# Kernel tuning notes

Hardware: AMD Instinct MI355X
Metric: run time of the kernel (lower is better)

Reference implementation:

```python
import jax, jax.numpy as jnp
import numpy as np

B, NX, NY = 16, 1024, 1024
DIN_X, DIN_Y = 768, 283
DK, DV, NH = 80, 80, 8
HK, HV = DK // NH, DV // NH  # 10, 10
NORM = 1.0 / np.sqrt(HK)


def setup_inputs() -> dict:
    key = jax.random.key(0)
    kx, ky, kq, kk, kv = jax.random.split(key, 5)
    x = jax.random.normal(kx, (B, NX, DIN_X), dtype=jnp.float32)
    y = jax.random.normal(ky, (B, NY, DIN_Y), dtype=jnp.float32)
    attn_mask = jnp.zeros((B, NX, NY), dtype=jnp.float32)  # unused in forward (dead arg in original)
    # torch nn.Linear weights are [out, in]; kaiming-uniform-ish init scale
    Wq = jax.random.normal(kq, (DK, DIN_X), dtype=jnp.float32) / np.sqrt(DIN_X)
    Wk = jax.random.normal(kk, (DK, DIN_Y), dtype=jnp.float32) / np.sqrt(DIN_Y)
    Wv = jax.random.normal(kv, (DV, DIN_Y), dtype=jnp.float32) / np.sqrt(DIN_Y)
    return {"x": x, "y": y, "attn_mask": attn_mask, "Wq": Wq, "Wk": Wk, "Wv": Wv}


def reference(x, y, attn_mask, Wq, Wk, Wv):
    b, n_x, _ = x.shape
    n_y = y.shape[1]
    # projections (Linear, no bias): [B,N,D] @ W^T
    q = (x @ Wq.T).reshape(b, n_x, NH, HK).transpose(0, 2, 1, 3)  # [B,H,Nx,hk]
    k = (y @ Wk.T).reshape(b, n_y, NH, HK).transpose(0, 2, 1, 3)  # [B,H,Ny,hk]
    v = (y @ Wv.T).reshape(b, n_y, NH, HV).transpose(0, 2, 1, 3)  # [B,H,Ny,hv]
    scores = jnp.einsum("bhqd,bhkd->bhqk", q, k) * NORM          # [B,H,Nx,Ny]
    dist = jax.nn.softmax(scores, axis=-1)
    # dropout p=0.5 is identity in eval mode
    att = jnp.einsum("bhqk,bhkd->bhqd", dist, v)                  # [B,H,Nx,hv]
    att = att.transpose(0, 2, 1, 3).reshape(b, n_x, DV)           # [B,Nx,dim_v]
    return att, dist
```

## Files before the change

kernel.cpp:

```cpp
#include <hip/hip_runtime.h>
#include <hip/hip_bf16.h>

#define BB 16
#define NXX 1024
#define NYY 1024
#define DINX 768
#define DINY 283
#define NHH 8
#define HKK 10
#define DKV 80
#define NORMF 0.31622776601683794f

#define NP 1310720UL
#define NR2 4194304UL


__device__ __forceinline__ float dot10(const float* a, const float* b) {
  float s = a[0] * b[0];
#pragma unroll
  for (int d = 1; d < 10; ++d) s = fmaf(a[d], b[d], s);
  return s;
}

__global__ __launch_bounds__(256) void proj_q(
    const float* __restrict__ X, const float* __restrict__ Wq, float* __restrict__ Pq) {
  __shared__ float Xs[64 * 33];
  const int t = threadIdx.x;
  const int rt = blockIdx.x >> 2;
  const int ks = blockIdx.x & 3;
  const int w = __builtin_amdgcn_readfirstlane(t >> 6);
  const int lane = t & 63;
  const int cbase = w * 20;
  const int kbase = ks * 192;

  float acc[20];
#pragma unroll
  for (int c = 0; c < 20; ++c) acc[c] = 0.f;

#pragma unroll 1
  for (int ch = 0; ch < 6; ++ch) {
    const int dk = kbase + ch * 32;
    __syncthreads();
    for (int u = t; u < 2048; u += 256) {
      const int r = u >> 5, c = u & 31;
      Xs[r * 33 + c] = X[(size_t)(rt * 64 + r) * DINX + dk + c];
    }
    __syncthreads();
    float xv[32];
#pragma unroll
    for (int k = 0; k < 32; ++k) xv[k] = Xs[lane * 33 + k];
#pragma unroll
    for (int c = 0; c < 20; ++c) {
      const float* wr = Wq + (size_t)(cbase + c) * DINX + dk;
#pragma unroll
      for (int k = 0; k < 32; ++k) acc[c] = fmaf(wr[k], xv[k], acc[c]);
    }
  }

  const int row = rt * 64 + lane;
  const int b = row >> 10, n = row & 1023;
  float* dst = Pq + (size_t)ks * NP;
#pragma unroll
  for (int c = 0; c < 20; ++c) {
    const int cc = cbase + c, h = cc / 10, d = cc - 10 * h;
    dst[(((size_t)b * NHH + h) * 1024 + n) * 10 + d] = acc[c];
  }
}

__global__ __launch_bounds__(512) void proj_kv(
    const float* __restrict__ Y, const float* __restrict__ WK, const float* __restrict__ WV,
    float* __restrict__ PKd, float* __restrict__ PKr) {
  __shared__ float Xs[64 * 33];
  const int t = threadIdx.x;
  const int rt = blockIdx.x >> 1;
  const int ks = blockIdx.x & 1;
  const int w = __builtin_amdgcn_readfirstlane(t >> 6);
  const int lane = t & 63;
  const bool isV = (w >= 4);
  const int cbase = (isV ? (w - 4) : w) * 20;
  const float* W = isV ? WV : WK;
  const int kbase = ks * 160;
  const int nch = ks ? 4 : 5;

  float acc[20];
#pragma unroll
  for (int c = 0; c < 20; ++c) acc[c] = 0.f;

#pragma unroll 1
  for (int ch = 0; ch < nch; ++ch) {
    const int dk = kbase + ch * 32;
    __syncthreads();
    for (int u = t; u < 2048; u += 512) {
      const int r = u >> 5, c = u & 31;
      const int d = dk + c;
      Xs[r * 33 + c] = (d < DINY) ? Y[(size_t)(rt * 64 + r) * DINY + d] : 0.f;
    }
    __syncthreads();
    float xv[32];
#pragma unroll
    for (int k = 0; k < 32; ++k) xv[k] = Xs[lane * 33 + k];
    if (dk + 32 <= DINY) {
#pragma unroll
      for (int c = 0; c < 20; ++c) {
        const float* wr = W + (size_t)(cbase + c) * DINY + dk;
#pragma unroll
        for (int k = 0; k < 32; ++k) acc[c] = fmaf(wr[k], xv[k], acc[c]);
      }
    } else {
#pragma unroll
      for (int c = 0; c < 20; ++c) {
        const float* wr = W + (size_t)(cbase + c) * DINY + dk;
#pragma unroll
        for (int k = 0; k < 27; ++k) acc[c] = fmaf(wr[k], xv[k], acc[c]);
      }
    }
  }

  const int row = rt * 64 + lane;
  const int b = row >> 10, n = row & 1023;
#pragma unroll
  for (int c = 0; c < 20; ++c) {
    const int cc = cbase + c, h = cc / 10, d = cc - 10 * h;
    const size_t bh = (size_t)b * NHH + h;
    const size_t grow = bh * 1024 + n;
    if (!isV) {
      const float v = acc[c] * NORMF;
      PKd[(size_t)ks * NP + (bh * 5 + (d >> 1)) * 2048 + n * 2 + (d & 1)] = v;
      PKr[(size_t)ks * NR2 + grow * 32 + d] = v;
    } else {
      PKr[(size_t)ks * NR2 + grow * 32 + 16 + d] = acc[c];
    }
  }
}

__global__ __launch_bounds__(256) void reduce_k(const float* __restrict__ ws, float* __restrict__ F) {
  const int NIQ = NP / 4;
  const int NIK = NP / 4;
  const int NIR = NR2 / 4;
  const float4* w4 = (const float4*)ws;
  float4* F4 = (float4*)F;
  const int total = NIQ + NIK + NIR;
  for (int i = blockIdx.x * 256 + threadIdx.x; i < total; i += gridDim.x * 256) {
    float4 s;
    if (i < NIQ) {
      const float4* P = w4;
      float4 a = P[i], b = P[i + NIQ], c = P[i + 2 * NIQ], d = P[i + 3 * NIQ];
      s.x = a.x + b.x + c.x + d.x; s.y = a.y + b.y + c.y + d.y;
      s.z = a.z + b.z + c.z + d.z; s.w = a.w + b.w + c.w + d.w;
      F4[i] = s;
    } else if (i < NIQ + NIK) {
      const int j = i - NIQ;
      const float4* P = w4 + 4 * NIQ;
      float4 a = P[j], b = P[j + NIK];
      s.x = a.x + b.x; s.y = a.y + b.y; s.z = a.z + b.z; s.w = a.w + b.w;
      F4[i] = s;
    } else {
      const int j = i - NIQ - NIK;
      const float4* P = w4 + 6 * NIQ;
      float4 a = P[j], b = P[j + NIR];
      s.x = a.x + b.x; s.y = a.y + b.y; s.z = a.z + b.z; s.w = a.w + b.w;
      F4[i] = s;
    }
  }
}

__global__ __launch_bounds__(64) void attn_kernel(
    const float* __restrict__ Qhm, const float* __restrict__ Kdm,
    const float* __restrict__ KVr, float* __restrict__ out_att,
    float* __restrict__ out_dist) {
  __shared__ float qs[64 * 12];

  const int lane = threadIdx.x;
  const int bid = blockIdx.x;
  const int nt = bid & 15;
  const int bh = bid >> 4;
  const int n = nt * 64 + lane;

  float qr[10];
  {
    const float2* qp = (const float2*)(Qhm + ((size_t)bh * 1024 + n) * 10);
#pragma unroll
    for (int dd = 0; dd < 5; ++dd) {
      float2 v = qp[dd];
      qr[2 * dd] = v.x; qr[2 * dd + 1] = v.y;
    }
  }

  float acc[10];
#pragma unroll
  for (int d = 0; d < 10; ++d) acc[d] = 0.f;
  float l = 0.f;

  const float4* kv4 = (const float4*)(KVr + (size_t)bh * 1024 * 32);
#pragma unroll 2
  for (int k = 0; k < 1024; ++k) {
    const float4* rec = kv4 + (size_t)k * 8;
    float4 a0 = rec[0], a1 = rec[1], a2 = rec[2];
    float kf[10] = {a0.x, a0.y, a0.z, a0.w, a1.x, a1.y, a1.z, a1.w, a2.x, a2.y};
    const float p = __expf(dot10(qr, kf));
    l += p;
    float4 b0 = rec[4], b1 = rec[5], b2 = rec[6];
    float vf[10] = {b0.x, b0.y, b0.z, b0.w, b1.x, b1.y, b1.z, b1.w, b2.x, b2.y};
#pragma unroll
    for (int d = 0; d < 10; ++d) acc[d] = fmaf(p, vf[d], acc[d]);
  }

  const float rl = 1.0f / l;
  {
    float* ap = out_att + ((size_t)(bh >> 3) * 1024 + n) * DKV + (bh & 7) * HKK;
#pragma unroll
    for (int dd = 0; dd < 5; ++dd)
      *(float2*)&ap[2 * dd] = make_float2(acc[2 * dd] * rl, acc[2 * dd + 1] * rl);
  }
#pragma unroll
  for (int d = 0; d < 10; ++d) qs[lane * 12 + d] = qr[d];
  qs[lane * 12 + 10] = rl;
  __syncthreads();

  const float4* kp4 = (const float4*)(Kdm + (size_t)bh * 10240);
  float* drow = out_dist + ((size_t)bh * 1024 + (size_t)nt * 64) * 1024;
#pragma unroll 1
  for (int c = 0; c < 8; ++c) {
    const int kb = c * 128 + lane * 2;
    float kA[10], kB[10];
#pragma unroll
    for (int dp = 0; dp < 5; ++dp) {
      float4 v = kp4[dp * 512 + (kb >> 1)];
      kA[2 * dp] = v.x; kA[2 * dp + 1] = v.y;
      kB[2 * dp] = v.z; kB[2 * dp + 1] = v.w;
    }
#pragma unroll 4
    for (int qq = 0; qq < 64; ++qq) {
      float4 qa = *(const float4*)&qs[qq * 12];
      float4 qb = *(const float4*)&qs[qq * 12 + 4];
      float4 qc = *(const float4*)&qs[qq * 12 + 8];
      float qv[10] = {qa.x, qa.y, qa.z, qa.w, qb.x, qb.y, qb.z, qb.w, qc.x, qc.y};
      const float rlq = qc.z;
      const float p0 = __expf(dot10(qv, kA)) * rlq;
      const float p1 = __expf(dot10(qv, kB)) * rlq;
      *(float2*)&drow[(size_t)qq * 1024 + kb] = make_float2(p0, p1);
    }
  }
}

extern "C" void kernel_launch(void* const* d_in, const int* in_sizes, int n_in,
                              void* d_out, int out_size, void* d_ws, size_t ws_size,
                              hipStream_t stream) {
  (void)in_sizes; (void)n_in; (void)out_size; (void)ws_size;
  const float* x = (const float*)d_in[0];
  const float* y = (const float*)d_in[1];
  const float* Wq = (const float*)d_in[3];
  const float* Wk = (const float*)d_in[4];
  const float* Wv = (const float*)d_in[5];

  float* out = (float*)d_out;
  float* att_out = out;
  float* dist_out = out + (size_t)BB * NXX * DKV;

  float* ws = (float*)d_ws;
  float* Pq  = ws;
  float* PKd = ws + 4 * NP;
  float* PKr = ws + 6 * NP;
  float* F   = ws + 8 * NP + 2 * NR2;
  float* Qhm = F;
  float* Kdm = F + NP;
  float* KVr = F + 2 * NP;

  proj_q<<<1024, 256, 0, stream>>>(x, Wq, Pq);
  proj_kv<<<512, 512, 0, stream>>>(y, Wk, Wv, PKd, PKr);
  reduce_k<<<2048, 256, 0, stream>>>(ws, F);
  attn_kernel<<<BB * NHH * 16, 64, 0, stream>>>(Qhm, Kdm, KVr, att_out, dist_out);
}
```

Baseline: 543.5 us.

## Split attention into split-K row-sum kernel and separate dist-writing kernel

The single 64-thread attention kernel is split in two. The first uses 256 threads per block, with four waves each covering a quarter of the keys, and reduces the partial sums through shared memory before writing att and the per-row q plus reciprocal sum to workspace. The second kernel writes the dist matrix with 256 threads, each computing four columns and storing float4s. This is meant to raise occupancy and parallelism over the serial 1024-key loop and widen the stores, at the cost of an extra launch and a round trip through global memory for q and the reciprocal.

```diff
diff --git a/kernel.cpp b/kernel.cpp
--- a/kernel.cpp
+++ b/kernel.cpp
@@ -164,17 +164,19 @@
   }
 }
 
-__global__ __launch_bounds__(64) void attn_kernel(
-    const float* __restrict__ Qhm, const float* __restrict__ Kdm,
-    const float* __restrict__ KVr, float* __restrict__ out_att,
-    float* __restrict__ out_dist) {
-  __shared__ float qs[64 * 12];
-
-  const int lane = threadIdx.x;
+__global__ __launch_bounds__(256) void attn_lv(
+    const float* __restrict__ Qhm, const float* __restrict__ KVr,
+    float* __restrict__ out_att, float* __restrict__ qrl) {
+  __shared__ float pl[4][64];
+  __shared__ float pa[4][64][10];
+
+  const int t = threadIdx.x;
+  const int w = __builtin_amdgcn_readfirstlane(t >> 6);
+  const int lane = t & 63;
   const int bid = blockIdx.x;
-  const int nt = bid & 15;
+  const int qt = bid & 15;
   const int bh = bid >> 4;
-  const int n = nt * 64 + lane;
+  const int n = qt * 64 + lane;
 
   float qr[10];
   {
@@ -191,9 +193,9 @@
   for (int d = 0; d < 10; ++d) acc[d] = 0.f;
   float l = 0.f;
 
-  const float4* kv4 = (const float4*)(KVr + (size_t)bh * 1024 * 32);
+  const float4* kv4 = (const float4*)(KVr + (size_t)bh * 32768) + (size_t)w * 256 * 8;
 #pragma unroll 2
-  for (int k = 0; k < 1024; ++k) {
+  for (int k = 0; k < 256; ++k) {
     const float4* rec = kv4 + (size_t)k * 8;
     float4 a0 = rec[0], a1 = rec[1], a2 = rec[2];
     float kf[10] = {a0.x, a0.y, a0.z, a0.w, a1.x, a1.y, a1.z, a1.w, a2.x, a2.y};
@@ -205,41 +207,69 @@
     for (int d = 0; d < 10; ++d) acc[d] = fmaf(p, vf[d], acc[d]);
   }
 
-  const float rl = 1.0f / l;
-  {
+  pl[w][lane] = l;
+#pragma unroll
+  for (int d = 0; d < 10; ++d) pa[w][lane][d] = acc[d];
+  __syncthreads();
+
+  if (w == 0) {
+    float L = pl[0][lane] + pl[1][lane] + pl[2][lane] + pl[3][lane];
+    float a[10];
+#pragma unroll
+    for (int d = 0; d < 10; ++d)
+      a[d] = pa[0][lane][d] + pa[1][lane][d] + pa[2][lane][d] + pa[3][lane][d];
+    const float rl = 1.0f / L;
     float* ap = out_att + ((size_t)(bh >> 3) * 1024 + n) * DKV + (bh & 7) * HKK;
 #pragma unroll
     for (int dd = 0; dd < 5; ++dd)
-      *(float2*)&ap[2 * dd] = make_float2(acc[2 * dd] * rl, acc[2 * dd + 1] * rl);
-  }
-#pragma unroll
-  for (int d = 0; d < 10; ++d) qs[lane * 12 + d] = qr[d];
-  qs[lane * 12 + 10] = rl;
-  __syncthreads();
-
+      *(float2*)&ap[2 * dd] = make_float2(a[2 * dd] * rl, a[2 * dd + 1] * rl);
+    float* qo = qrl + ((size_t)bh * 1024 + n) * 12;
+#pragma unroll
+    for (int d = 0; d < 10; ++d) qo[d] = qr[d];
+    qo[10] = rl;
+    qo[11] = 0.f;
+  }
+}
+
+__global__ __launch_bounds__(256) void attn_dist(
+    const float* __restrict__ Kdm, const float* __restrict__ qrl,
+    float* __restrict__ out_dist) {
+  const int t = threadIdx.x;
+  const int w = __builtin_amdgcn_readfirstlane(t >> 6);
+  const int lane = t & 63;
+  const int bid = blockIdx.x;
+  const int qt = bid & 15;
+  const int bh = bid >> 4;
+
+  const int kb = w * 256 + lane * 4;
   const float4* kp4 = (const float4*)(Kdm + (size_t)bh * 10240);
-  float* drow = out_dist + ((size_t)bh * 1024 + (size_t)nt * 64) * 1024;
-#pragma unroll 1
-  for (int c = 0; c < 8; ++c) {
-    const int kb = c * 128 + lane * 2;
-    float kA[10], kB[10];
-#pragma unroll
-    for (int dp = 0; dp < 5; ++dp) {
-      float4 v = kp4[dp * 512 + (kb >> 1)];
-      kA[2 * dp] = v.x; kA[2 * dp + 1] = v.y;
-      kB[2 * dp] = v.z; kB[2 * dp + 1] = v.w;
-    }
-#pragma unroll 4
-    for (int qq = 0; qq < 64; ++qq) {
-      float4 qa = *(const float4*)&qs[qq * 12];
-      float4 qb = *(const float4*)&qs[qq * 12 + 4];
-      float4 qc = *(const float4*)&qs[qq * 12 + 8];
-      float qv[10] = {qa.x, qa.y, qa.z, qa.w, qb.x, qb.y, qb.z, qb.w, qc.x, qc.y};
-      const float rlq = qc.z;
-      const float p0 = __expf(dot10(qv, kA)) * rlq;
-      const float p1 = __expf(dot10(qv, kB)) * rlq;
-      *(float2*)&drow[(size_t)qq * 1024 + kb] = make_float2(p0, p1);
-    }
+  float kA[10], kB[10], kC[10], kD[10];
+#pragma unroll
+  for (int dp = 0; dp < 5; ++dp) {
+    float4 va = kp4[dp * 512 + (kb >> 1)];
+    float4 vb = kp4[dp * 512 + (kb >> 1) + 1];
+    kA[2 * dp] = va.x; kA[2 * dp + 1] = va.y;
+    kB[2 * dp] = va.z; kB[2 * dp + 1] = va.w;
+    kC[2 * dp] = vb.x; kC[2 * dp + 1] = vb.y;
+    kD[2 * dp] = vb.z; kD[2 * dp + 1] = vb.w;
+  }
+
+  const float* qbase = qrl + ((size_t)bh * 1024 + qt * 64) * 12;
+  float* drow = out_dist + ((size_t)bh * 1024 + qt * 64) * 1024 + kb;
+#pragma unroll 2
+  for (int qq = 0; qq < 64; ++qq) {
+    const float* qp = qbase + qq * 12;
+    float4 qa = *(const float4*)qp;
+    float4 qb = *(const float4*)(qp + 4);
+    float4 qc = *(const float4*)(qp + 8);
+    float qv[10] = {qa.x, qa.y, qa.z, qa.w, qb.x, qb.y, qb.z, qb.w, qc.x, qc.y};
+    const float rlq = qc.z;
+    float4 o;
+    o.x = __expf(dot10(qv, kA)) * rlq;
+    o.y = __expf(dot10(qv, kB)) * rlq;
+    o.z = __expf(dot10(qv, kC)) * rlq;
+    o.w = __expf(dot10(qv, kD)) * rlq;
+    *(float4*)&drow[(size_t)qq * 1024] = o;
   }
 }
 
@@ -265,9 +295,11 @@
   float* Qhm = F;
   float* Kdm = F + NP;
   float* KVr = F + 2 * NP;
+  float* qrl = F + 2 * NP + NR2;
 
   proj_q<<<1024, 256, 0, stream>>>(x, Wq, Pq);
   proj_kv<<<512, 512, 0, stream>>>(y, Wk, Wv, PKd, PKr);
   reduce_k<<<2048, 256, 0, stream>>>(ws, F);
-  attn_kernel<<<BB * NHH * 16, 64, 0, stream>>>(Qhm, Kdm, KVr, att_out, dist_out);
-}
+  attn_lv<<<BB * NHH * 16, 256, 0, stream>>>(Qhm, KVr, att_out, qrl);
+  attn_dist<<<BB * NHH * 16, 256, 0, stream>>>(Kdm, qrl, dist_out);
+}
```

After: 484.9 us. 10.8% less time.
